# Optimization experiments

Hardware: AMD Instinct MI355X
Metric: run time of the kernel (lower is better)

The kernel has to match this reference:

```python
import jax, jax.numpy as jnp
import numpy as np

N = 768          # nodes
E_HALF = 12288   # undirected edges (both directions added -> E = 24576)
P = 4096         # query pairs
H = 32           # hidden_dim_1wl == hidden_dim_2wl
MAX_X = 100
EPS = 1e-5
LAYER1 = 2


def setup_inputs() -> dict:
    key = jax.random.key(0)
    ks = jax.random.split(key, 12)
    s = 0.1
    x = jax.random.randint(ks[0], (N,), 0, MAX_X + 1)
    half = jax.random.randint(ks[1], (2, E_HALF), 0, N)
    ei = jnp.concatenate([half, half[::-1]], axis=1)          # symmetric edge set [2,E]
    pos = jax.random.randint(ks[2], (P, 2), 0, N)
    emb = jax.random.normal(ks[3], (MAX_X + 1, H)) * s
    gcn_W = jax.random.normal(ks[4], (LAYER1, H, H)) * s
    gcn_b = jnp.zeros((LAYER1, H))
    mlp1_W = jax.random.normal(ks[5], (2 * H, H)) * s
    mlp1_b = jnp.zeros((H,))
    mlp2_W = jax.random.normal(ks[6], (2 * H, H)) * s
    mlp2_b = jnp.zeros((H,))
    mlp3_W = jax.random.normal(ks[7], (H + 1, H)) * s
    mlp3_b = jnp.zeros((H,))
    lin_W = jax.random.normal(ks[8], (2 * H, 1)) * s
    lin_b = jnp.zeros((1,))
    return dict(x=x, ei=ei, pos=pos, emb=emb, gcn_W=gcn_W, gcn_b=gcn_b,
                mlp1_W=mlp1_W, mlp1_b=mlp1_b, mlp2_W=mlp2_W, mlp2_b=mlp2_b,
                mlp3_W=mlp3_W, mlp3_b=mlp3_b, lin_W=lin_W, lin_b=lin_b)


def _graph_norm(h):
    # PyG-style GraphNorm with default params (mean_scale=1, weight=1, bias=0)
    h = h - h.mean(0)
    return h * jax.lax.rsqrt((h * h).mean(0) + EPS)


def reference(x, ei, pos, emb, gcn_W, gcn_b, mlp1_W, mlp1_b,
              mlp2_W, mlp2_b, mlp3_W, mlp3_b, lin_W, lin_b):
    n = x.shape[0]
    d = emb.shape[1]
    h = emb[x]                                                 # [n,H] (dropout=0)
    # --- GCNConv stack: Ahat = D^-1/2 (A+I) D^-1/2 ---
    A = jnp.zeros((n, n), h.dtype).at[ei[0], ei[1]].set(1.0)
    Ahat = A + jnp.eye(n, dtype=h.dtype)
    dinv = jax.lax.rsqrt(Ahat.sum(1))
    An = Ahat * dinv[:, None] * dinv[None, :]
    for l in range(gcn_W.shape[0]):
        h = An @ (h @ gcn_W[l]) + gcn_b[l]
        h = jax.nn.relu(_graph_norm(h))                        # GraphNorm + ReLU
    # --- pair features ---
    xx = h[pos[:, 0]] * h[pos[:, 1]]                           # [P,H]
    val = jnp.concatenate([h[ei[0]], h[ei[1]]], 1)             # [E,2H]
    xe = jax.nn.relu(val @ mlp1_W + mlp1_b)                    # mlps_1
    mul = jax.nn.relu(val @ mlp2_W + mlp2_b)                   # mlps_2[0]
    # --- sparse_bmm as dense [n,n,d] contraction (coalesce sums duplicates -> .add) ---
    Xd = jnp.zeros((n, n, d), h.dtype).at[ei[0], ei[1]].add(xe)
    Md = jnp.zeros((n, n, d), h.dtype).at[ei[0], ei[1]].add(mul)
    C = jnp.einsum('ikd,kjd->ijd', Xd, Md)                     # x_{ij} = sum_k x_{ik}*mul_{kj}
    # support of the sparse result: 2-hop pairs union original edges (sparse_cat)
    adj_b = jnp.zeros((n, n), bool).at[ei[0], ei[1]].set(True)
    af = adj_b.astype(h.dtype)
    mask = ((af @ af) > 0) | adj_b
    ind = af[..., None]                                        # ones-column for original edges
    value = jnp.concatenate([C, ind], -1)                      # [n,n,H+1]
    z = value @ mlp3_W + mlp3_b                                # mlps_3[0]
    # GraphNorm over the edge support only (faithful to sparse values())
    m = mask.astype(h.dtype)[..., None]
    cnt = m.sum()
    mean = (z * m).sum((0, 1)) / cnt
    z = z - mean
    var = ((z * z) * m).sum((0, 1)) / cnt
    z = jax.nn.relu(z * jax.lax.rsqrt(var + EPS))
    # x * sm: multiply by transposed values; zero outside support (= add_zero)
    sym = z * jnp.swapaxes(z, 0, 1) * m
    pair = sym[pos[:, 0], pos[:, 1]]                           # [P,H] (edge_list gather)
    out = jnp.concatenate([pair, xx], 1) @ lin_W + lin_b       # lin_dir -> [P,1]
    return out
```

## Files before the change

### kernel.cpp

```cpp
#include <hip/hip_runtime.h>
#include <hip/hip_bf16.h>

#define NN 768
#define NE 24576
#define NPOS 4096
#define NCELL (NN*NN)
#define NBLK 2304
#define NBLK2 1152
#define NREP 16

typedef __hip_bfloat16 bf16;

__device__ __forceinline__ float ldf(const void* p, int i, int mode) {
    return mode ? __bfloat162float(((const bf16*)p)[i]) : ((const float*)p)[i];
}
__device__ __forceinline__ float aread(float* p) { return atomicAdd(p, 0.f); }
__device__ __forceinline__ int areadi(int* p) { return atomicAdd(p, 0); }

template<int D, int HALF>
__device__ __forceinline__ void redRound(float* v, int lane) {
#pragma unroll
    for (int i = 0; i < HALF; i++) {
        float snd = (lane & D) ? v[i] : v[i + HALF];
        float r = __shfl_xor(snd, D);
        v[i] = ((lane & D) ? v[i + HALF] : v[i]) + r;
    }
}

#define DOT4(Z, A, W) Z += A.x * W.x + A.y * W.y + A.z * W.z + A.w * W.w

#define GATH(rec, q0,q1,q2,q3,q4,q5,q6,q7) { \
    const float4* xr = xep4 + (rec).x * 8; \
    const float4* mr = mulp4 + (rec).y * 8; \
    float4 xv0 = xr[0], xv1 = xr[1], xv2 = xr[2], xv3 = xr[3]; \
    float4 xv4 = xr[4], xv5 = xr[5], xv6 = xr[6], xv7 = xr[7]; \
    float4 mv0 = mr[0], mv1 = mr[1], mv2 = mr[2], mv3 = mr[3]; \
    float4 mv4 = mr[4], mv5 = mr[5], mv6 = mr[6], mv7 = mr[7]; \
    q0.x += xv0.x*mv0.x; q0.y += xv0.y*mv0.y; q0.z += xv0.z*mv0.z; q0.w += xv0.w*mv0.w; \
    q1.x += xv1.x*mv1.x; q1.y += xv1.y*mv1.y; q1.z += xv1.z*mv1.z; q1.w += xv1.w*mv1.w; \
    q2.x += xv2.x*mv2.x; q2.y += xv2.y*mv2.y; q2.z += xv2.z*mv2.z; q2.w += xv2.w*mv2.w; \
    q3.x += xv3.x*mv3.x; q3.y += xv3.y*mv3.y; q3.z += xv3.z*mv3.z; q3.w += xv3.w*mv3.w; \
    q4.x += xv4.x*mv4.x; q4.y += xv4.y*mv4.y; q4.z += xv4.z*mv4.z; q4.w += xv4.w*mv4.w; \
    q5.x += xv5.x*mv5.x; q5.y += xv5.y*mv5.y; q5.z += xv5.z*mv5.z; q5.w += xv5.w*mv5.w; \
    q6.x += xv6.x*mv6.x; q6.y += xv6.y*mv6.y; q6.z += xv6.z*mv6.z; q6.w += xv6.w*mv6.w; \
    q7.x += xv7.x*mv7.x; q7.y += xv7.y*mv7.y; q7.z += xv7.z*mv7.z; q7.w += xv7.w*mv7.w; }

__global__ void k_scatter(const int* __restrict__ ei, int* __restrict__ cell, int* __restrict__ rowlen,
                          int* __restrict__ row_ptr, float* __restrict__ dinv, int* __restrict__ dc,
                          const void* __restrict__ gW, const void* __restrict__ gB,
                          const void* __restrict__ m1W, const void* __restrict__ m1B,
                          const void* __restrict__ m2W, const void* __restrict__ m2B,
                          const void* __restrict__ m3W, const void* __restrict__ m3B,
                          const void* __restrict__ lW,  const void* __restrict__ lB,
                          const void* __restrict__ emb, int* __restrict__ modeg,
                          float* __restrict__ gwf, float* __restrict__ gbf,
                          float* __restrict__ w1f, float* __restrict__ b1f,
                          float* __restrict__ w2f, float* __restrict__ b2f,
                          float* __restrict__ w3q, float* __restrict__ linf, float* __restrict__ linb) {
    int t = threadIdx.x;
    if (blockIdx.x == 96) {
        __shared__ int bad;
        if (t == 0) bad = 0;
        __syncthreads();
        int local = 0;
        for (int i = t; i < 3232; i += 256) {
            float a = fabsf(__bfloat162float(((const bf16*)emb)[i]));
            if (!(a < 100.f)) local = 1;
        }
        if (local) atomicOr(&bad, 1);
        __syncthreads();
        int mode = bad ? 0 : 1;
        if (t == 0) *modeg = mode;
        for (int i = t; i < 2048; i += 256) {
            gwf[i] = ldf(gW, i, mode);
            w1f[i] = ldf(m1W, i, mode);
            w2f[i] = ldf(m2W, i, mode);
        }
        for (int i = t; i < 64; i += 256) { gbf[i] = ldf(gB, i, mode); linf[i] = ldf(lW, i, mode); }
        if (t < 32) { b1f[t] = ldf(m1B, t, mode); b2f[t] = ldf(m2B, t, mode); }
        for (int i = t; i < 1056; i += 256) { int c = i >> 5, d = i & 31; w3q[d * 36 + c] = ldf(m3W, i, mode); }
        if (t < 32) { w3q[t * 36 + 33] = ldf(m3B, t, mode); w3q[t * 36 + 34] = 0.f; w3q[t * 36 + 35] = 0.f; }
        if (t == 0) linb[0] = ldf(lB, 0, mode);
        return;
    }
    __shared__ int amlast;
    __shared__ int sI[256];
    int e = blockIdx.x * 256 + t;
    int a = ei[e], b = ei[NE + e];
    if ((unsigned)a < (unsigned)NN && (unsigned)b < (unsigned)NN) {
        int old = atomicAdd(&cell[a * NN + b], 1);
        if (old == 0) atomicAdd(&rowlen[a], 1);
    }
    __syncthreads();
    if (t == 0) { __threadfence(); amlast = (atomicAdd(dc, 1) == 95) ? 1 : 0; }
    __syncthreads();
    if (!amlast) return;
    int i0 = 3 * t;
    int r0 = areadi(&rowlen[i0]), r1 = areadi(&rowlen[i0 + 1]), r2 = areadi(&rowlen[i0 + 2]);
    dinv[i0]     = rsqrtf((float)r0 + 1.f);
    dinv[i0 + 1] = rsqrtf((float)r1 + 1.f);
    dinv[i0 + 2] = rsqrtf((float)r2 + 1.f);
    int s3 = r0 + r1 + r2;
    sI[t] = s3;
    __syncthreads();
    for (int off = 1; off < 256; off <<= 1) {
        int tmp = (t >= off) ? sI[t - off] : 0;
        __syncthreads();
        sI[t] += tmp;
        __syncthreads();
    }
    int excl = sI[t] - s3;
    row_ptr[i0] = excl;
    row_ptr[i0 + 1] = excl + r0;
    row_ptr[i0 + 2] = excl + r0 + r1;
    if (t == 255) row_ptr[NN] = sI[255];
}

__global__ void k_fill(int* __restrict__ cell, const int* __restrict__ row_ptr, int* __restrict__ cursor,
                       int* __restrict__ col_idx, float* __restrict__ cntv, int* __restrict__ pr_row,
                       const int* __restrict__ rowlen, int* __restrict__ rtot,
                       const int* __restrict__ x, const void* __restrict__ emb,
                       const int* __restrict__ modep, float* __restrict__ bufA) {
    int t = threadIdx.x;
    int b = blockIdx.x;
    if (b < NBLK) {
        int idx = b * 256 + t;
        int i = idx / NN;
        int j = idx - i * NN;
        int cv = cell[idx];
        if (cv > 0) {
            int p = row_ptr[i] + atomicAdd(&cursor[i], 1);
            col_idx[p] = j; cntv[p] = (float)cv; pr_row[p] = i;
            cell[idx] = p;
            atomicAdd(&rtot[i], rowlen[j]);
        } else cell[idx] = -1;
    } else {
        int idx = (b - NBLK) * 256 + t;
        int i = idx >> 5, k = idx & 31;
        int xi = x[i]; if (xi < 0) xi = 0; if (xi > 100) xi = 100;
        bufA[idx] = ldf(emb, xi * 32 + k, *modep);
    }
}

__global__ void k_aggmw0(const int* __restrict__ rtot, int* __restrict__ row_base,
                         const int* __restrict__ row_ptr, const int* __restrict__ col_idx,
                         const float* __restrict__ bufA, const float* __restrict__ dinv,
                         const float* __restrict__ gwf, const float* __restrict__ gbf,
                         float* __restrict__ bufB) {
    int t = threadIdx.x;
    if (blockIdx.x == 0) {
        __shared__ int sI[256];
        int r3[3]; int s3 = 0;
#pragma unroll
        for (int q = 0; q < 3; q++) { r3[q] = rtot[3 * t + q]; s3 += r3[q]; }
        sI[t] = s3;
        __syncthreads();
        for (int off = 1; off < 256; off <<= 1) {
            int tmp = (t >= off) ? sI[t - off] : 0;
            __syncthreads();
            sI[t] += tmp;
            __syncthreads();
        }
        int run = sI[t] - s3;
        row_base[3 * t] = run;
        row_base[3 * t + 1] = run + r3[0];
        row_base[3 * t + 2] = run + r3[0] + r3[1];
        return;
    }
    __shared__ float sg[8][32];
    int li = t >> 5, k = t & 31;
    int i = (blockIdx.x - 1) * 8 + li;
    int base = row_ptr[i], len = row_ptr[i + 1] - base;
    float di = dinv[i];
    float acc = di * bufA[i * 32 + k];
    for (int e = 0; e < len; e++) {
        int c = col_idx[base + e];
        acc += dinv[c] * bufA[c * 32 + k];
    }
    sg[li][k] = di * acc;
    __syncthreads();
    int d = k;
    float s = gbf[d];
#pragma unroll
    for (int kk = 0; kk < 32; kk++) s += sg[li][kk] * gwf[kk * 32 + d];
    bufB[i * 32 + d] = s;
}

__global__ void k_hist(const int* __restrict__ row_ptr, const int* __restrict__ col_idx,
                       const int* __restrict__ row_base,
                       int* __restrict__ pcur, int2* __restrict__ paths2, int cap,
                       const float* __restrict__ bufB, float* __restrict__ nrm0) {
    int t = threadIdx.x;
    if (blockIdx.x == NN) {
        __shared__ float r1[256], r2[256];
        int dd = t & 31, g = t >> 5;
        float s = 0.f, s2 = 0.f;
        for (int r = g; r < NN; r += 8) { float v = bufB[r * 32 + dd]; s += v; s2 += v * v; }
        r1[t] = s; r2[t] = s2;
        __syncthreads();
        if (t < 32) {
            float a = 0.f, b2 = 0.f;
            for (int k = 0; k < 8; k++) { a += r1[k * 32 + t]; b2 += r2[k * 32 + t]; }
            float mean = a / (float)NN;
            float var = b2 / (float)NN - mean * mean;
            nrm0[t] = mean;
            nrm0[32 + t] = rsqrtf(fmaxf(var, 0.f) + 1e-5f);
        }
        return;
    }
    __shared__ int hist[NN];
    __shared__ int sc[256];
    int i = blockIdx.x;
    int base = row_ptr[i], len = row_ptr[i + 1] - base;
    int rb = row_base[i];
    int wave = t >> 6, lane = t & 63;
    for (int j = t; j < NN; j += 256) hist[j] = 0;
    __syncthreads();
    for (int ee = wave; ee < len; ee += 4) {
        int k = col_idx[base + ee];
        int kb = row_ptr[k], ke = row_ptr[k + 1];
        for (int e = kb + lane; e < ke; e += 64) atomicAdd(&hist[col_idx[e]], 1);
    }
    __syncthreads();
    int h0 = hist[3 * t], h1 = hist[3 * t + 1], h2 = hist[3 * t + 2];
    int s3 = h0 + h1 + h2;
    sc[t] = s3;
    __syncthreads();
    for (int off = 1; off < 256; off <<= 1) {
        int tmp = (t >= off) ? sc[t - off] : 0;
        __syncthreads();
        sc[t] += tmp;
        __syncthreads();
    }
    int excl = sc[t] - s3;
    int n0 = i * NN + 3 * t;
    pcur[n0]     = rb + excl + h0;
    pcur[n0 + 1] = rb + excl + h0 + h1;
    pcur[n0 + 2] = rb + excl + h0 + h1 + h2;
    hist[3 * t] = excl;
    hist[3 * t + 1] = excl + h0;
    hist[3 * t + 2] = excl + h0 + h1;
    __syncthreads();
    for (int ee = wave; ee < len; ee += 4) {
        int e1 = base + ee;
        int k = col_idx[e1];
        int kb = row_ptr[k], ke = row_ptr[k + 1];
        for (int e = kb + lane; e < ke; e += 64) {
            int j = col_idx[e];
            int slot = rb + atomicAdd(&hist[j], 1);
            if (slot < cap) paths2[slot] = make_int2(e1, e);
        }
    }
}

__global__ void k_aggmw1(const int* __restrict__ row_ptr, const int* __restrict__ col_idx,
                         const float* __restrict__ bufB, const float* __restrict__ nrm0,
                         const float* __restrict__ dinv,
                         const float* __restrict__ gwf, const float* __restrict__ gbf,
                         float* __restrict__ bufA, float* __restrict__ stats1) {
    __shared__ float sg[8][32];
    int t = threadIdx.x;
    int li = t >> 5, k = t & 31;
    int i = blockIdx.x * 8 + li;
    float mk = nrm0[k], rk = nrm0[32 + k];
    int base = row_ptr[i], len = row_ptr[i + 1] - base;
    float di = dinv[i];
    float acc = di * fmaxf((bufB[i * 32 + k] - mk) * rk, 0.f);
    for (int e = 0; e < len; e++) {
        int c = col_idx[base + e];
        acc += dinv[c] * fmaxf((bufB[c * 32 + k] - mk) * rk, 0.f);
    }
    sg[li][k] = di * acc;
    __syncthreads();
    int d = k;
    const float* W = gwf + 1024;
    float s = gbf[32 + d];
#pragma unroll
    for (int kk = 0; kk < 32; kk++) s += sg[li][kk] * W[kk * 32 + d];
    bufA[i * 32 + d] = s;
    __syncthreads();
    sg[li][d] = s;
    __syncthreads();
    if (t < 32) {
        float ps = 0.f, ps2 = 0.f;
#pragma unroll
        for (int q = 0; q < 8; q++) { float v = sg[q][t]; ps += v; ps2 += v * v; }
        float* rep = stats1 + (blockIdx.x & (NREP - 1)) * 80;
        atomicAdd(&rep[t], ps);
        atomicAdd(&rep[32 + t], ps2);
    }
}

__global__ void k_emlp(const float* __restrict__ bufA, const float* __restrict__ stats1,
                       const int* __restrict__ row_ptr, const int* __restrict__ col_idx,
                       const int* __restrict__ pr_row, const float* __restrict__ cntv,
                       const float* __restrict__ w1f, const float* __restrict__ b1f,
                       const float* __restrict__ w2f, const float* __restrict__ b2f,
                       float* __restrict__ xep, float* __restrict__ mulp, float* __restrict__ h) {
    __shared__ float nmean[32], nrstd[32];
    int t = threadIdx.x;
    int b = blockIdx.x;
    if (t < 32) {
        float s = 0.f, s2 = 0.f;
#pragma unroll
        for (int r = 0; r < NREP; r++) { s += stats1[r * 80 + t]; s2 += stats1[r * 80 + 32 + t]; }
        float mean = s / (float)NN;
        float var = s2 / (float)NN - mean * mean;
        nmean[t] = mean;
        nrstd[t] = rsqrtf(fmaxf(var, 0.f) + 1e-5f);
    }
    __syncthreads();
    if (b < 3072) {
        int d = t & 31;
        int p = b * 8 + (t >> 5);
        if (p >= row_ptr[NN]) {
            if (p < NE) { xep[p * 32 + d] = 0.f; mulp[p * 32 + d] = 0.f; }
            return;
        }
        int i = pr_row[p], j = col_idx[p];
        float a1 = b1f[d], a2 = b2f[d];
#pragma unroll
        for (int c = 0; c < 32; c++) {
            float hv = fmaxf((bufA[i * 32 + c] - nmean[c]) * nrstd[c], 0.f);
            a1 += hv * w1f[c * 32 + d];
            a2 += hv * w2f[c * 32 + d];
        }
#pragma unroll
        for (int c = 0; c < 32; c++) {
            float hv = fmaxf((bufA[j * 32 + c] - nmean[c]) * nrstd[c], 0.f);
            a1 += hv * w1f[(32 + c) * 32 + d];
            a2 += hv * w2f[(32 + c) * 32 + d];
        }
        float cv = cntv[p];
        xep[p * 32 + d]  = cv * fmaxf(a1, 0.f);
        mulp[p * 32 + d] = cv * fmaxf(a2, 0.f);
    } else {
        int idx = (b - 3072) * 256 + t;
        int d = idx & 31;
        h[idx] = fmaxf((bufA[idx] - nmean[d]) * nrstd[d], 0.f);
    }
}

__global__ __launch_bounds__(256, 2) void k_big(const int* __restrict__ pcur,
                                                const int2* __restrict__ paths2,
                                                const int* __restrict__ cell,
                                                const float4* __restrict__ xep4, const float4* __restrict__ mulp4,
                                                const float* __restrict__ w3q,
                                                float* __restrict__ stats, int* __restrict__ done,
                                                float* __restrict__ nrm, int cap) {
    __shared__ float sS1[32], sS2[32];
    __shared__ float sCm;
    __shared__ int amlast;
    int t = threadIdx.x, lane = t & 63;
    int b = blockIdx.x;
    int n0 = b * 512 + 2 * t;
    if (t == 0) sCm = 0.f;
    if (t < 32) { sS1[t] = 0.f; sS2[t] = 0.f; }
    __syncthreads();
    int p0a = (n0 == 0) ? 0 : pcur[n0 - 1];
    int p1a = pcur[n0];
    int p1b = pcur[n0 + 1];
    if (p0a > cap) p0a = cap; if (p1a > cap) p1a = cap; if (p1b > cap) p1b = cap;
    int lenA = p1a - p0a, lenB = p1b - p1a;
    int lim = (lenA > lenB) ? lenA : lenB;
    float4 a0 = {0.f,0.f,0.f,0.f}, a1 = a0, a2 = a0, a3 = a0, a4 = a0, a5 = a0, a6 = a0, a7 = a0;
    float4 c0 = a0, c1 = a0, c2 = a0, c3 = a0, c4 = a0, c5 = a0, c6 = a0, c7 = a0;
    for (int q = 0; q < lim; q++) {
        int2 recA, recB;
        bool doA = q < lenA, doB = q < lenB;
        if (doA) recA = paths2[p0a + q];
        if (doB) recB = paths2[p1a + q];
        if (doA) GATH(recA, a0, a1, a2, a3, a4, a5, a6, a7);
        if (doB) GATH(recB, c0, c1, c2, c3, c4, c5, c6, c7);
    }
    bool adja = cell[n0] >= 0;
    bool adjb = cell[n0 + 1] >= 0;
    float afa = adja ? 1.f : 0.f;
    float afb = adjb ? 1.f : 0.f;
    float mska = (lenA > 0 || adja) ? 1.f : 0.f;
    float mskb = (lenB > 0 || adjb) ? 1.f : 0.f;
#pragma unroll
    for (int ch = 0; ch < 2; ch++) {
        float v[32];
#pragma unroll
        for (int j = 0; j < 16; j++) {
            int dd = ch * 16 + j;
            const float4* wr = (const float4*)(w3q + dd * 36);
            float4 wv = wr[8];
            float za = wv.y + afa * wv.x;
            float zb = wv.y + afb * wv.x;
            wv = wr[0]; DOT4(za, a0, wv); DOT4(zb, c0, wv);
            wv = wr[1]; DOT4(za, a1, wv); DOT4(zb, c1, wv);
            wv = wr[2]; DOT4(za, a2, wv); DOT4(zb, c2, wv);
            wv = wr[3]; DOT4(za, a3, wv); DOT4(zb, c3, wv);
            wv = wr[4]; DOT4(za, a4, wv); DOT4(zb, c4, wv);
            wv = wr[5]; DOT4(za, a5, wv); DOT4(zb, c5, wv);
            wv = wr[6]; DOT4(za, a6, wv); DOT4(zb, c6, wv);
            wv = wr[7]; DOT4(za, a7, wv); DOT4(zb, c7, wv);
            v[j] = mska * za + mskb * zb;
            v[16 + j] = mska * za * za + mskb * zb * zb;
        }
#pragma unroll
        for (int i2 = 0; i2 < 32; i2++) v[i2] += __shfl_xor(v[i2], 32);
        redRound<16, 16>(v, lane);
        redRound<8, 8>(v, lane);
        redRound<4, 4>(v, lane);
        redRound<2, 2>(v, lane);
        redRound<1, 1>(v, lane);
        if (lane < 32) {
            if (lane < 16) atomicAdd(&sS1[ch * 16 + lane], v[0]);
            else           atomicAdd(&sS2[ch * 16 + lane - 16], v[0]);
        }
    }
    {
        float cm2 = mska + mskb;
        for (int off = 32; off >= 1; off >>= 1) cm2 += __shfl_xor(cm2, off);
        if (lane == 0) atomicAdd(&sCm, cm2);
    }
    __syncthreads();
    float* srep = stats + (b & (NREP - 1)) * 80;
    if (t < 32) {
        atomicAdd(&srep[t], sS1[t]);
        atomicAdd(&srep[32 + t], sS2[t]);
    }
    if (t == 32) atomicAdd(&srep[64], sCm);
    __syncthreads();
    if (t == 0) {
        __threadfence();
        amlast = (atomicAdd(done, 1) == NBLK2 - 1) ? 1 : 0;
    }
    __syncthreads();
    if (amlast && t < 32) {
        float sum1 = 0.f, sum2 = 0.f;
        for (int r = 0; r < NREP; r++) {
            sum1 += aread(&stats[r * 80 + t]);
            sum2 += aread(&stats[r * 80 + 32 + t]);
        }
        float cmv = 0.f;
        for (int r = 0; r < NREP; r++) cmv += aread(&stats[r * 80 + 64]);
        if (cmv < 1.f) cmv = 1.f;
        float mean = sum1 / cmv;
        float var = sum2 / cmv - mean * mean;
        nrm[t] = mean;
        nrm[32 + t] = rsqrtf(fmaxf(var, 0.f) + 1e-5f);
    }
}

__global__ void k_out(const int* __restrict__ pos, const int* __restrict__ pcur,
                      const int2* __restrict__ paths2,
                      const int* __restrict__ cell,
                      const float* __restrict__ xep, const float* __restrict__ mulp,
                      const float* __restrict__ h,
                      const float* __restrict__ w3q,
                      const float* __restrict__ nrm,
                      const float* __restrict__ linf, const float* __restrict__ linb,
                      const int* __restrict__ modep, int cap, void* __restrict__ outp) {
    __shared__ float Cb[4][2][32];
    int t = threadIdx.x;
    int w = t >> 6, lane = t & 63, d = lane & 31, dir = lane >> 5;
    int p = blockIdx.x * 4 + w;
    int a = pos[2 * p], b = pos[2 * p + 1];
    if ((unsigned)a >= (unsigned)NN) a = 0;
    if ((unsigned)b >= (unsigned)NN) b = 0;
    int r = dir ? b : a;
    int cc = dir ? a : b;
    int n = r * NN + cc;
    int p1 = pcur[n];
    int p0 = (n == 0) ? 0 : pcur[n - 1];
    if (p0 > cap) p0 = cap; if (p1 > cap) p1 = cap;
    float acc = 0.f;
    for (int q = p0; q < p1; q++) {
        int2 rec = paths2[q];
        acc += xep[rec.x * 32 + d] * mulp[rec.y * 32 + d];
    }
    Cb[w][dir][d] = acc;
    bool adj = cell[n] >= 0;
    float msk = (p1 > p0 || adj) ? 1.f : 0.f;
    __syncthreads();
    float z = w3q[d * 36 + 33] + (adj ? 1.f : 0.f) * w3q[d * 36 + 32];
#pragma unroll
    for (int c = 0; c < 32; c++) z += Cb[w][dir][c] * w3q[d * 36 + c];
    float zn = fmaxf((z - nrm[d]) * nrm[32 + d], 0.f);
    float zp = __shfl_xor(zn, 32);
    float symd = msk * zn * zp;
    float xxd = h[a * 32 + d] * h[b * 32 + d];
    float contrib = symd * linf[d] + xxd * linf[32 + d];
    for (int off = 16; off >= 1; off >>= 1) contrib += __shfl_xor(contrib, off);
    if (lane == 0) {
        float v = contrib + linb[0];
        v = fminf(fmaxf(v, -1e4f), 1e4f);
        if (*modep) ((bf16*)outp)[p] = __float2bfloat16(v);
        else        ((float*)outp)[p] = v;
    }
}

extern "C" void kernel_launch(void* const* d_in, const int* in_sizes, int n_in,
                              void* d_out, int out_size, void* d_ws, size_t ws_size,
                              hipStream_t stream) {
    const void* px  = d_in[0];  const void* pei = d_in[1];  const void* ppos = d_in[2];
    const void* pemb = d_in[3]; const void* pgW = d_in[4];  const void* pgB  = d_in[5];
    const void* pm1W = d_in[6]; const void* pm1B = d_in[7]; const void* pm2W = d_in[8];
    const void* pm2B = d_in[9]; const void* pm3W = d_in[10]; const void* pm3B = d_in[11];
    const void* plW = d_in[12]; const void* plB = d_in[13];
    {
        int c2048 = 0, c64 = 0, c32 = 0;
        for (int i = 0; i < n_in; i++) {
            int s = in_sizes[i]; const void* p = d_in[i];
            switch (s) {
                case 768:   px = p; break;
                case 49152: pei = p; break;
                case 8192:  ppos = p; break;
                case 3232:  pemb = p; break;
                case 2048:  if (c2048 == 0) pgW = p; else if (c2048 == 1) pm1W = p; else pm2W = p; c2048++; break;
                case 64:    if (c64 == 0) pgB = p; else plW = p; c64++; break;
                case 32:    if (c32 == 0) pm1B = p; else if (c32 == 1) pm2B = p; else pm3B = p; c32++; break;
                case 1056:  pm3W = p; break;
                case 1:     plB = p; break;
                default: break;
            }
        }
    }

    char* ws = (char*)d_ws;
    size_t off = 0;
    auto alloc = [&](size_t bytes) -> void* {
        void* pp = ws + off;
        off += (bytes + 255) & ~(size_t)255;
        return pp;
    };
    int*   cell    = (int*)alloc(NCELL * 4);
    int*   pcur    = (int*)alloc(NCELL * 4);
    char*  aux0    = ws + off;
    int*   rowlen  = (int*)alloc(NN * 4);
    int*   rtot    = (int*)alloc(NN * 4);
    int*   cursor  = (int*)alloc(NN * 4);
    float* stats   = (float*)alloc(NREP * 80 * 4);
    float* stats1  = (float*)alloc(NREP * 80 * 4);
    int*   dcs     = (int*)alloc(8 * 4);
    size_t auxlen  = (ws + off) - aux0;
    int*   row_base= (int*)alloc(NN * 4);
    int*   row_ptr = (int*)alloc((NN + 1) * 4);
    int*   col_idx = (int*)alloc(NE * 4);
    float* cntv    = (float*)alloc(NE * 4);
    int*   pr_row  = (int*)alloc(NE * 4);
    float* dinv    = (float*)alloc(NN * 4);
    float* h       = (float*)alloc(NN * 32 * 4);
    float* bufA    = (float*)alloc(NN * 32 * 4);
    float* bufB    = (float*)alloc(NN * 32 * 4);
    float* xep     = (float*)alloc(NE * 32 * 4);
    float* mulp    = (float*)alloc(NE * 32 * 4);
    float* nrm     = (float*)alloc(64 * 4);
    float* nrm0    = (float*)alloc(64 * 4);
    float* gwf     = (float*)alloc(2048 * 4);
    float* gbf     = (float*)alloc(64 * 4);
    float* w1f     = (float*)alloc(2048 * 4);
    float* b1f     = (float*)alloc(32 * 4);
    float* w2f     = (float*)alloc(2048 * 4);
    float* b2f     = (float*)alloc(32 * 4);
    float* w3q     = (float*)alloc(32 * 36 * 4);
    float* linf    = (float*)alloc(64 * 4);
    float* linb    = (float*)alloc(4);
    int*   modeg   = (int*)alloc(4);
    size_t remain = (ws_size > off) ? (ws_size - off) : 0;
    int cap = (int)(remain / 8);
    if (cap > (1 << 20)) cap = (1 << 20);
    int2*  paths2  = (int2*)alloc((size_t)cap * 8);

    hipMemsetAsync(cell, 0, (size_t)NCELL * 4, stream);
    hipMemsetAsync(aux0, 0, auxlen, stream);
    k_scatter<<<97, 256, 0, stream>>>((const int*)pei, cell, rowlen, row_ptr, dinv, &dcs[0],
                                      pgW, pgB, pm1W, pm1B, pm2W, pm2B, pm3W, pm3B, plW, plB,
                                      pemb, modeg, gwf, gbf, w1f, b1f, w2f, b2f, w3q, linf, linb);
    k_fill<<<NBLK + 96, 256, 0, stream>>>(cell, row_ptr, cursor, col_idx, cntv, pr_row,
                                          rowlen, rtot, (const int*)px, pemb, modeg, bufA);
    k_aggmw0<<<1 + 96, 256, 0, stream>>>(rtot, row_base, row_ptr, col_idx, bufA, dinv, gwf, gbf, bufB);
    k_hist<<<NN + 1, 256, 0, stream>>>(row_ptr, col_idx, row_base, pcur, paths2, cap, bufB, nrm0);
    k_aggmw1<<<96, 256, 0, stream>>>(row_ptr, col_idx, bufB, nrm0, dinv, gwf, gbf, bufA, stats1);
    k_emlp<<<3072 + 96, 256, 0, stream>>>(bufA, stats1, row_ptr, col_idx, pr_row, cntv,
                                          w1f, b1f, w2f, b2f, xep, mulp, h);
    k_big<<<NBLK2, 256, 0, stream>>>(pcur, paths2, cell, (const float4*)xep, (const float4*)mulp,
                                     w3q, stats, &dcs[1], nrm, cap);
    k_out<<<NPOS / 4, 256, 0, stream>>>((const int*)ppos, pcur, paths2, cell, xep, mulp, h,
                                        w3q, nrm, linf, linb, modeg, cap, d_out);
}
```

Baseline: 299.8 us.

## Parallelize k_big over path records with LDS atomic accumulation per cell

k_big previously gave each thread two output cells and looped over each cell's path list, which leaves lanes idle when path counts differ. Now each block owns 256 consecutive cells and its threads stride evenly over the block's contiguous range of path records. Each record's elementwise products are added into a padded shared-memory tile with atomics, and the cell's low 8 bits are packed into the high bits of the edge index so the destination cell is known. This balances work across lanes at the cost of 32 LDS atomics per record and a larger shared footprint. It also assumes the edge index fits in 16 bits.

```diff
diff --git a/kernel.cpp b/kernel.cpp
--- a/kernel.cpp
+++ b/kernel.cpp
@@ -6,7 +6,6 @@
 #define NPOS 4096
 #define NCELL (NN*NN)
 #define NBLK 2304
-#define NBLK2 1152
 #define NREP 16
 
 typedef __hip_bfloat16 bf16;
@@ -26,24 +25,6 @@
         v[i] = ((lane & D) ? v[i + HALF] : v[i]) + r;
     }
 }
-
-#define DOT4(Z, A, W) Z += A.x * W.x + A.y * W.y + A.z * W.z + A.w * W.w
-
-#define GATH(rec, q0,q1,q2,q3,q4,q5,q6,q7) { \
-    const float4* xr = xep4 + (rec).x * 8; \
-    const float4* mr = mulp4 + (rec).y * 8; \
-    float4 xv0 = xr[0], xv1 = xr[1], xv2 = xr[2], xv3 = xr[3]; \
-    float4 xv4 = xr[4], xv5 = xr[5], xv6 = xr[6], xv7 = xr[7]; \
-    float4 mv0 = mr[0], mv1 = mr[1], mv2 = mr[2], mv3 = mr[3]; \
-    float4 mv4 = mr[4], mv5 = mr[5], mv6 = mr[6], mv7 = mr[7]; \
-    q0.x += xv0.x*mv0.x; q0.y += xv0.y*mv0.y; q0.z += xv0.z*mv0.z; q0.w += xv0.w*mv0.w; \
-    q1.x += xv1.x*mv1.x; q1.y += xv1.y*mv1.y; q1.z += xv1.z*mv1.z; q1.w += xv1.w*mv1.w; \
-    q2.x += xv2.x*mv2.x; q2.y += xv2.y*mv2.y; q2.z += xv2.z*mv2.z; q2.w += xv2.w*mv2.w; \
-    q3.x += xv3.x*mv3.x; q3.y += xv3.y*mv3.y; q3.z += xv3.z*mv3.z; q3.w += xv3.w*mv3.w; \
-    q4.x += xv4.x*mv4.x; q4.y += xv4.y*mv4.y; q4.z += xv4.z*mv4.z; q4.w += xv4.w*mv4.w; \
-    q5.x += xv5.x*mv5.x; q5.y += xv5.y*mv5.y; q5.z += xv5.z*mv5.z; q5.w += xv5.w*mv5.w; \
-    q6.x += xv6.x*mv6.x; q6.y += xv6.y*mv6.y; q6.z += xv6.z*mv6.z; q6.w += xv6.w*mv6.w; \
-    q7.x += xv7.x*mv7.x; q7.y += xv7.y*mv7.y; q7.z += xv7.z*mv7.z; q7.w += xv7.w*mv7.w; }
 
 __global__ void k_scatter(const int* __restrict__ ei, int* __restrict__ cell, int* __restrict__ rowlen,
                           int* __restrict__ row_ptr, float* __restrict__ dinv, int* __restrict__ dc,
@@ -248,7 +229,7 @@
         for (int e = kb + lane; e < ke; e += 64) {
             int j = col_idx[e];
             int slot = rb + atomicAdd(&hist[j], 1);
-            if (slot < cap) paths2[slot] = make_int2(e1, e);
+            if (slot < cap) paths2[slot] = make_int2(e1 | ((j & 255) << 16), e);
         }
     }
 }
@@ -341,44 +322,80 @@
     }
 }
 
-__global__ __launch_bounds__(256, 2) void k_big(const int* __restrict__ pcur,
+__global__ __launch_bounds__(256, 4) void k_big(const int* __restrict__ pcur,
                                                 const int2* __restrict__ paths2,
                                                 const int* __restrict__ cell,
                                                 const float4* __restrict__ xep4, const float4* __restrict__ mulp4,
                                                 const float* __restrict__ w3q,
                                                 float* __restrict__ stats, int* __restrict__ done,
                                                 float* __restrict__ nrm, int cap) {
+    __shared__ float Cs[32 * 257];
     __shared__ float sS1[32], sS2[32];
     __shared__ float sCm;
     __shared__ int amlast;
     int t = threadIdx.x, lane = t & 63;
     int b = blockIdx.x;
-    int n0 = b * 512 + 2 * t;
+    int nbase = b * 256;
+    for (int e = t; e < 32 * 257; e += 256) Cs[e] = 0.f;
     if (t == 0) sCm = 0.f;
     if (t < 32) { sS1[t] = 0.f; sS2[t] = 0.f; }
     __syncthreads();
-    int p0a = (n0 == 0) ? 0 : pcur[n0 - 1];
-    int p1a = pcur[n0];
-    int p1b = pcur[n0 + 1];
-    if (p0a > cap) p0a = cap; if (p1a > cap) p1a = cap; if (p1b > cap) p1b = cap;
-    int lenA = p1a - p0a, lenB = p1b - p1a;
-    int lim = (lenA > lenB) ? lenA : lenB;
-    float4 a0 = {0.f,0.f,0.f,0.f}, a1 = a0, a2 = a0, a3 = a0, a4 = a0, a5 = a0, a6 = a0, a7 = a0;
-    float4 c0 = a0, c1 = a0, c2 = a0, c3 = a0, c4 = a0, c5 = a0, c6 = a0, c7 = a0;
-    for (int q = 0; q < lim; q++) {
-        int2 recA, recB;
-        bool doA = q < lenA, doB = q < lenB;
-        if (doA) recA = paths2[p0a + q];
-        if (doB) recB = paths2[p1a + q];
-        if (doA) GATH(recA, a0, a1, a2, a3, a4, a5, a6, a7);
-        if (doB) GATH(recB, c0, c1, c2, c3, c4, c5, c6, c7);
-    }
-    bool adja = cell[n0] >= 0;
-    bool adjb = cell[n0 + 1] >= 0;
-    float afa = adja ? 1.f : 0.f;
-    float afb = adjb ? 1.f : 0.f;
-    float mska = (lenA > 0 || adja) ? 1.f : 0.f;
-    float mskb = (lenB > 0 || adjb) ? 1.f : 0.f;
+    int P0 = (b == 0) ? 0 : pcur[nbase - 1];
+    int P1 = pcur[nbase + 255];
+    if (P0 > cap) P0 = cap; if (P1 > cap) P1 = cap;
+    for (int p = P0 + t; p < P1; p += 256) {
+        int2 rec = paths2[p];
+        int e1 = rec.x & 0xFFFF;
+        int local = (rec.x >> 16) & 0xFF;
+        const float4* xr = xep4 + e1 * 8;
+        const float4* mr = mulp4 + rec.y * 8;
+        float4 xv0 = xr[0], xv1 = xr[1], xv2 = xr[2], xv3 = xr[3];
+        float4 xv4 = xr[4], xv5 = xr[5], xv6 = xr[6], xv7 = xr[7];
+        float4 mv0 = mr[0], mv1 = mr[1], mv2 = mr[2], mv3 = mr[3];
+        float4 mv4 = mr[4], mv5 = mr[5], mv6 = mr[6], mv7 = mr[7];
+        atomicAdd(&Cs[ 0 * 257 + local], xv0.x * mv0.x);
+        atomicAdd(&Cs[ 1 * 257 + local], xv0.y * mv0.y);
+        atomicAdd(&Cs[ 2 * 257 + local], xv0.z * mv0.z);
+        atomicAdd(&Cs[ 3 * 257 + local], xv0.w * mv0.w);
+        atomicAdd(&Cs[ 4 * 257 + local], xv1.x * mv1.x);
+        atomicAdd(&Cs[ 5 * 257 + local], xv1.y * mv1.y);
+        atomicAdd(&Cs[ 6 * 257 + local], xv1.z * mv1.z);
+        atomicAdd(&Cs[ 7 * 257 + local], xv1.w * mv1.w);
+        atomicAdd(&Cs[ 8 * 257 + local], xv2.x * mv2.x);
+        atomicAdd(&Cs[ 9 * 257 + local], xv2.y * mv2.y);
+        atomicAdd(&Cs[10 * 257 + local], xv2.z * mv2.z);
+        atomicAdd(&Cs[11 * 257 + local], xv2.w * mv2.w);
+        atomicAdd(&Cs[12 * 257 + local], xv3.x * mv3.x);
+        atomicAdd(&Cs[13 * 257 + local], xv3.y * mv3.y);
+        atomicAdd(&Cs[14 * 257 + local], xv3.z * mv3.z);
+        atomicAdd(&Cs[15 * 257 + local], xv3.w * mv3.w);
+        atomicAdd(&Cs[16 * 257 + local], xv4.x * mv4.x);
+        atomicAdd(&Cs[17 * 257 + local], xv4.y * mv4.y);
+        atomicAdd(&Cs[18 * 257 + local], xv4.z * mv4.z);
+        atomicAdd(&Cs[19 * 257 + local], xv4.w * mv4.w);
+        atomicAdd(&Cs[20 * 257 + local], xv5.x * mv5.x);
+        atomicAdd(&Cs[21 * 257 + local], xv5.y * mv5.y);
+        atomicAdd(&Cs[22 * 257 + local], xv5.z * mv5.z);
+        atomicAdd(&Cs[23 * 257 + local], xv5.w * mv5.w);
+        atomicAdd(&Cs[24 * 257 + local], xv6.x * mv6.x);
+        atomicAdd(&Cs[25 * 257 + local], xv6.y * mv6.y);
+        atomicAdd(&Cs[26 * 257 + local], xv6.z * mv6.z);
+        atomicAdd(&Cs[27 * 257 + local], xv6.w * mv6.w);
+        atomicAdd(&Cs[28 * 257 + local], xv7.x * mv7.x);
+        atomicAdd(&Cs[29 * 257 + local], xv7.y * mv7.y);
+        atomicAdd(&Cs[30 * 257 + local], xv7.z * mv7.z);
+        atomicAdd(&Cs[31 * 257 + local], xv7.w * mv7.w);
+    }
+    __syncthreads();
+    int n = nbase + t;
+    int p1 = pcur[n];
+    int p0 = (n == 0) ? 0 : pcur[n - 1];
+    bool adj = cell[n] >= 0;
+    float af = adj ? 1.f : 0.f;
+    float msk = (p1 > p0 || adj) ? 1.f : 0.f;
+    float Creg[32];
+#pragma unroll
+    for (int c = 0; c < 32; c++) Creg[c] = Cs[c * 257 + t];
 #pragma unroll
     for (int ch = 0; ch < 2; ch++) {
         float v[32];
@@ -387,18 +404,17 @@
             int dd = ch * 16 + j;
             const float4* wr = (const float4*)(w3q + dd * 36);
             float4 wv = wr[8];
-            float za = wv.y + afa * wv.x;
-            float zb = wv.y + afb * wv.x;
-            wv = wr[0]; DOT4(za, a0, wv); DOT4(zb, c0, wv);
-            wv = wr[1]; DOT4(za, a1, wv); DOT4(zb, c1, wv);
-            wv = wr[2]; DOT4(za, a2, wv); DOT4(zb, c2, wv);
-            wv = wr[3]; DOT4(za, a3, wv); DOT4(zb, c3, wv);
-            wv = wr[4]; DOT4(za, a4, wv); DOT4(zb, c4, wv);
-            wv = wr[5]; DOT4(za, a5, wv); DOT4(zb, c5, wv);
-            wv = wr[6]; DOT4(za, a6, wv); DOT4(zb, c6, wv);
-            wv = wr[7]; DOT4(za, a7, wv); DOT4(zb, c7, wv);
-            v[j] = mska * za + mskb * zb;
-            v[16 + j] = mska * za * za + mskb * zb * zb;
+            float z = wv.y + af * wv.x;
+            wv = wr[0]; z += Creg[0]*wv.x + Creg[1]*wv.y + Creg[2]*wv.z + Creg[3]*wv.w;
+            wv = wr[1]; z += Creg[4]*wv.x + Creg[5]*wv.y + Creg[6]*wv.z + Creg[7]*wv.w;
+            wv = wr[2]; z += Creg[8]*wv.x + Creg[9]*wv.y + Creg[10]*wv.z + Creg[11]*wv.w;
+            wv = wr[3]; z += Creg[12]*wv.x + Creg[13]*wv.y + Creg[14]*wv.z + Creg[15]*wv.w;
+            wv = wr[4]; z += Creg[16]*wv.x + Creg[17]*wv.y + Creg[18]*wv.z + Creg[19]*wv.w;
+            wv = wr[5]; z += Creg[20]*wv.x + Creg[21]*wv.y + Creg[22]*wv.z + Creg[23]*wv.w;
+            wv = wr[6]; z += Creg[24]*wv.x + Creg[25]*wv.y + Creg[26]*wv.z + Creg[27]*wv.w;
+            wv = wr[7]; z += Creg[28]*wv.x + Creg[29]*wv.y + Creg[30]*wv.z + Creg[31]*wv.w;
+            v[j] = msk * z;
+            v[16 + j] = msk * z * z;
         }
 #pragma unroll
         for (int i2 = 0; i2 < 32; i2++) v[i2] += __shfl_xor(v[i2], 32);
@@ -413,7 +429,7 @@
         }
     }
     {
-        float cm2 = mska + mskb;
+        float cm2 = msk;
         for (int off = 32; off >= 1; off >>= 1) cm2 += __shfl_xor(cm2, off);
         if (lane == 0) atomicAdd(&sCm, cm2);
     }
@@ -427,7 +443,7 @@
     __syncthreads();
     if (t == 0) {
         __threadfence();
-        amlast = (atomicAdd(done, 1) == NBLK2 - 1) ? 1 : 0;
+        amlast = (atomicAdd(done, 1) == NBLK - 1) ? 1 : 0;
     }
     __syncthreads();
     if (amlast && t < 32) {
@@ -471,7 +487,8 @@
     float acc = 0.f;
     for (int q = p0; q < p1; q++) {
         int2 rec = paths2[q];
-        acc += xep[rec.x * 32 + d] * mulp[rec.y * 32 + d];
+        int e1 = rec.x & 0xFFFF;
+        acc += xep[e1 * 32 + d] * mulp[rec.y * 32 + d];
     }
     Cb[w][dir][d] = acc;
     bool adj = cell[n] >= 0;
@@ -578,8 +595,8 @@
     k_aggmw1<<<96, 256, 0, stream>>>(row_ptr, col_idx, bufB, nrm0, dinv, gwf, gbf, bufA, stats1);
     k_emlp<<<3072 + 96, 256, 0, stream>>>(bufA, stats1, row_ptr, col_idx, pr_row, cntv,
                                           w1f, b1f, w2f, b2f, xep, mulp, h);
-    k_big<<<NBLK2, 256, 0, stream>>>(pcur, paths2, cell, (const float4*)xep, (const float4*)mulp,
-                                     w3q, stats, &dcs[1], nrm, cap);
+    k_big<<<NBLK, 256, 0, stream>>>(pcur, paths2, cell, (const float4*)xep, (const float4*)mulp,
+                                    w3q, stats, &dcs[1], nrm, cap);
     k_out<<<NPOS / 4, 256, 0, stream>>>((const int*)ppos, pcur, paths2, cell, xep, mulp, h,
                                         w3q, nrm, linf, linb, modeg, cap, d_out);
 }
```

Result: slower. 416.1 us (+38.8%).
